# Kernel optimization log

Measured on AMD Instinct MI355X. Metric: run time of the kernel, lower is better.

## Reference

```python
import jax, jax.numpy as jnp
import numpy as np

D = 1024
H = 16
DH = D // H
SCALE = 1.0 / float(np.sqrt(DH))
EPS = 1e-5


def layer_norm(x, g, b):
    mu = jnp.mean(x, axis=-1, keepdims=True)
    var = jnp.mean((x - mu) ** 2, axis=-1, keepdims=True)
    return (x - mu) * jax.lax.rsqrt(var + EPS) * g + b


def setup_inputs() -> dict:
    key = jax.random.key(0)
    ks = jax.random.split(key, 12)
    B, N = 2, 2048
    x = jax.random.normal(ks[0], (B, N, D), dtype=jnp.float32)
    # sparse 0/1 adjacency (tree-like density) plus self loops
    adj = (jax.random.uniform(ks[1], (B, N, N)) < 0.002).astype(jnp.float32)
    adj = jnp.maximum(adj, jnp.eye(N, dtype=jnp.float32)[None])
    attn_mask = jnp.zeros((B, N, N), dtype=jnp.float32)
    s = 0.02
    params = {
        "qkv_w": jax.random.normal(ks[2], (D, 3 * D)) * s,
        "qkv_b": jnp.zeros((3 * D,), jnp.float32),
        "out_w": jax.random.normal(ks[3], (D, D)) * s,
        "out_b": jnp.zeros((D,), jnp.float32),
        "ln1_g": jnp.ones((D,), jnp.float32),
        "ln1_b": jnp.zeros((D,), jnp.float32),
        "ln2_g": jnp.ones((D,), jnp.float32),
        "ln2_b": jnp.zeros((D,), jnp.float32),
        "ff1_w": jax.random.normal(ks[4], (D, 4 * D)) * s,
        "ff1_b": jnp.zeros((4 * D,), jnp.float32),
        "ff2_w": jax.random.normal(ks[5], (4 * D, D)) * s,
        "ff2_b": jnp.zeros((D,), jnp.float32),
        "struct_bias": jnp.zeros((1,), jnp.float32) + 0.1,
    }
    return {"x": x, "adjacency": adj, "attn_mask": attn_mask, **params}


def reference(x, adjacency, attn_mask, qkv_w, qkv_b, out_w, out_b,
              ln1_g, ln1_b, ln2_g, ln2_b, ff1_w, ff1_b, ff2_w, ff2_b,
              struct_bias):
    b, n, d = x.shape
    residual = x
    h = layer_norm(x, ln1_g, ln1_b)
    qkv = (h @ qkv_w + qkv_b).reshape(b, n, 3, H, DH)
    q = jnp.transpose(qkv[:, :, 0], (0, 2, 1, 3))  # [B,H,N,Dh]
    k = jnp.transpose(qkv[:, :, 1], (0, 2, 1, 3))
    v = jnp.transpose(qkv[:, :, 2], (0, 2, 1, 3))
    scores = jnp.einsum("bhqd,bhkd->bhqk", q, k) * SCALE
    scores = scores + struct_bias[0] * adjacency[:, None] + attn_mask[:, None]
    attn = jax.nn.softmax(scores, axis=-1)  # dropout is identity at eval
    out = jnp.einsum("bhqk,bhkd->bhqd", attn, v)
    out = jnp.transpose(out, (0, 2, 1, 3)).reshape(b, n, d)
    out = out @ out_w + out_b
    x1 = residual + out
    h2 = layer_norm(x1, ln2_g, ln2_b)
    ff = jax.nn.gelu(h2 @ ff1_w + ff1_b, approximate=False) @ ff2_w + ff2_b
    return x1 + ff
```

## Files before the change

kernel.cpp:

```cpp
#include <hip/hip_runtime.h>
#include <math.h>

#define Dm 1024
#define Hh 16
#define DHh 64
#define Bb 2
#define Nn 2048
#define Rr 4096
#define SCALE_ 0.125f
#define EPS_ 1e-5f
#define SMAX_ 4.0f
#define LOG2E_ 1.4426950408889634f

typedef unsigned short u16;
typedef __attribute__((ext_vector_type(8))) short short8;
typedef __attribute__((ext_vector_type(4))) float f32x4;

__device__ __forceinline__ u16 f2bf(float f) {
  union { float f; unsigned u; } v; v.f = f;
  unsigned r = v.u + 0x7fffu + ((v.u >> 16) & 1u);
  return (u16)(r >> 16);
}
__device__ __forceinline__ u16 f2bf_t(float f) {
  union { float f; unsigned u; } v; v.f = f;
  return (u16)(v.u >> 16);
}
__device__ __forceinline__ float bf2f(u16 h) {
  union { unsigned u; float f; } v; v.u = ((unsigned)h) << 16;
  return v.f;
}

__device__ __forceinline__ void g2l16(const u16* g, const u16* l) {
  __builtin_amdgcn_global_load_lds(
      (const __attribute__((address_space(1))) void*)g,
      (__attribute__((address_space(3))) void*)l, 16, 0, 0);
}

__global__ void transpose_to_bf16(const float* __restrict__ W, u16* __restrict__ WT,
                                  int K, int N) {
  __shared__ float tile[32][33];
  int n0 = blockIdx.x * 32, k0 = blockIdx.y * 32;
  int tx = threadIdx.x, ty = threadIdx.y;
#pragma unroll
  for (int i = 0; i < 4; i++)
    tile[ty + 8 * i][tx] = W[(size_t)(k0 + ty + 8 * i) * N + n0 + tx];
  __syncthreads();
#pragma unroll
  for (int i = 0; i < 4; i++)
    WT[(size_t)(n0 + ty + 8 * i) * K + k0 + tx] = f2bf(tile[tx][ty + 8 * i]);
}

__global__ void bias_precompute(const float* __restrict__ adj, const float* __restrict__ mask,
                                const float* __restrict__ sbp, u16* __restrict__ bias16) {
  const float sb = sbp[0];
  size_t i = ((size_t)blockIdx.x * 256 + threadIdx.x) * 8;
  float4 a0 = *(const float4*)(adj + i);
  float4 a1 = *(const float4*)(adj + i + 4);
  float4 m0 = *(const float4*)(mask + i);
  float4 m1 = *(const float4*)(mask + i + 4);
  ushort4 o0, o1;
  o0.x = f2bf(sb * a0.x + m0.x); o0.y = f2bf(sb * a0.y + m0.y);
  o0.z = f2bf(sb * a0.z + m0.z); o0.w = f2bf(sb * a0.w + m0.w);
  o1.x = f2bf(sb * a1.x + m1.x); o1.y = f2bf(sb * a1.y + m1.y);
  o1.z = f2bf(sb * a1.z + m1.z); o1.w = f2bf(sb * a1.w + m1.w);
  *(ushort4*)(bias16 + i) = o0;
  *(ushort4*)(bias16 + i + 4) = o1;
}

template <int BI>
__global__ void ln_kernel(const void* __restrict__ xin, const float* __restrict__ g,
                          const float* __restrict__ be, u16* __restrict__ out) {
  int row = blockIdx.x;
  int t = threadIdx.x;
  float4 v;
  if (BI) {
    ushort4 uv = ((const ushort4*)((const u16*)xin + (size_t)row * Dm))[t];
    v.x = bf2f(uv.x); v.y = bf2f(uv.y); v.z = bf2f(uv.z); v.w = bf2f(uv.w);
  } else {
    v = ((const float4*)((const float*)xin + (size_t)row * Dm))[t];
  }
  float s = v.x + v.y + v.z + v.w;
  float s2 = v.x * v.x + v.y * v.y + v.z * v.z + v.w * v.w;
#pragma unroll
  for (int o = 32; o > 0; o >>= 1) { s += __shfl_down(s, o); s2 += __shfl_down(s2, o); }
  __shared__ float sm[8];
  int w = t >> 6;
  if ((t & 63) == 0) { sm[w] = s; sm[4 + w] = s2; }
  __syncthreads();
  if (t == 0) {
    float a = sm[0] + sm[1] + sm[2] + sm[3];
    float a2 = sm[4] + sm[5] + sm[6] + sm[7];
    float mu = a * (1.f / Dm);
    sm[0] = mu;
    sm[1] = rsqrtf(a2 * (1.f / Dm) - mu * mu + EPS_);
  }
  __syncthreads();
  float mu = sm[0], rstd = sm[1];
  float4 gv = ((const float4*)g)[t];
  float4 bv = ((const float4*)be)[t];
  ushort4 o4;
  o4.x = f2bf((v.x - mu) * rstd * gv.x + bv.x);
  o4.y = f2bf((v.y - mu) * rstd * gv.y + bv.y);
  o4.z = f2bf((v.z - mu) * rstd * gv.z + bv.z);
  o4.w = f2bf((v.w - mu) * rstd * gv.w + bv.w);
  ((ushort4*)(out + (size_t)row * Dm))[t] = o4;
}

template <int MODE, int MI, int NI>
__global__ __launch_bounds__(256) void gemm_bt(
    const u16* __restrict__ A, const u16* __restrict__ BT,
    const float* __restrict__ bias, const void* __restrict__ res,
    void* __restrict__ Cout, u16* __restrict__ qb,
    u16* __restrict__ kb, u16* __restrict__ vb, int Ndim, int Kdim) {
  constexpr int TM = MI * 32, TN = NI * 32;
  constexpr int NS = (TM + TN) / 16;
  __shared__ u16 As[2][TM * 32];
  __shared__ u16 Bs[2][TN * 32];
  const int t = threadIdx.x;
  const int wave = t >> 6, lane = t & 63;
  const int wm = wave >> 1, wn = wave & 1;
  const int lr = lane & 15, lq = lane >> 4;
  const int flat = blockIdx.x + gridDim.x * blockIdx.y;
  constexpr int nMb = 4096 / TM;
  constexpr int mpx = nMb / 8;
  const int xcd = flat & 7;
  const int p = flat >> 3;
  const int m0 = (xcd * mpx + (p % mpx)) * TM;
  const int n0 = (p / mpx) * TN;

  auto stage = [&](int kt, int bsel) {
    for (int s = wave; s < NS; s += 4) {
      if (s < TM / 16)
        g2l16(A + (size_t)(m0 + s * 16 + (lane >> 2)) * Kdim + kt + (lane & 3) * 8,
              &As[bsel][(s * 16) * 32]);
      else
        g2l16(BT + (size_t)(n0 + (s - TM / 16) * 16 + (lane >> 2)) * Kdim + kt + (lane & 3) * 8,
              &Bs[bsel][((s - TM / 16) * 16) * 32]);
    }
  };

  f32x4 acc[MI][NI];
#pragma unroll
  for (int i = 0; i < MI; i++)
#pragma unroll
    for (int j = 0; j < NI; j++) acc[i][j] = (f32x4){0.f, 0.f, 0.f, 0.f};

  stage(0, 0);
  int cur = 0;
  for (int kt = 0; kt < Kdim; kt += 32) {
    __syncthreads();
    if (kt + 32 < Kdim) stage(kt + 32, cur ^ 1);
    short8 af[MI], bf[NI];
#pragma unroll
    for (int i = 0; i < MI; i++)
      af[i] = *(const short8*)&As[cur][(wm * (MI * 16) + i * 16 + lr) * 32 + lq * 8];
#pragma unroll
    for (int j = 0; j < NI; j++)
      bf[j] = *(const short8*)&Bs[cur][(wn * (NI * 16) + j * 16 + lr) * 32 + lq * 8];
#pragma unroll
    for (int i = 0; i < MI; i++)
#pragma unroll
      for (int j = 0; j < NI; j++)
        acc[i][j] = __builtin_amdgcn_mfma_f32_16x16x32_bf16(af[i], bf[j], acc[i][j], 0, 0, 0);
    cur ^= 1;
  }

#pragma unroll
  for (int i = 0; i < MI; i++) {
#pragma unroll
    for (int j = 0; j < NI; j++) {
#pragma unroll
      for (int r = 0; r < 4; r++) {
        int row = m0 + wm * (MI * 16) + i * 16 + lq * 4 + r;
        int col = n0 + wn * (NI * 16) + j * 16 + lr;
        float val = acc[i][j][r] + bias[col];
        if (MODE == 0) {
          int s = col >> 10, rem = col & 1023;
          int hh = rem >> 6, dh = rem & 63;
          int bi = row >> 11, ni = row & 2047;
          if (s == 2) {
            vb[(((size_t)bi * Hh + hh) * DHh + dh) * Nn + ni] = f2bf(val);
          } else {
            u16* dst = (s == 0) ? qb : kb;
            dst[(((size_t)bi * Hh + hh) * Nn + ni) * DHh + dh] = f2bf(val);
          }
        } else if (MODE == 1) {
          size_t o = (size_t)row * Ndim + col;
          ((u16*)Cout)[o] = f2bf(val + ((const float*)res)[o]);
        } else if (MODE == 3) {
          size_t o = (size_t)row * Ndim + col;
          ((float*)Cout)[o] = val + bf2f(((const u16*)res)[o]);
        } else {
          size_t o = (size_t)row * Ndim + col;
          float gv = 0.5f * val * (1.f + erff(val * 0.70710678118f));
          ((u16*)Cout)[o] = f2bf(gv);
        }
      }
    }
  }
}

__global__ __launch_bounds__(256) void attn_kernel(
    const u16* __restrict__ q, const u16* __restrict__ k, const u16* __restrict__ vT,
    const u16* __restrict__ bias16, u16* __restrict__ out) {
  const int qt = blockIdx.x, hb = blockIdx.y;
  const int hh = hb & 15, b = hb >> 4;
  const int t = threadIdx.x, wave = t >> 6, lane = t & 63;
  const int lr = lane & 15, lq = lane >> 4;
  const size_t head_off = (((size_t)b * Hh + hh) * Nn) * DHh;
  const u16* Q = q + head_off;
  const u16* K = k + head_off;
  const u16* Vt = vT + head_off;
  const int q0 = qt * 128;

  __shared__ u16 Ks[64 * 72];
  __shared__ u16 VsT[64 * 72];
  __shared__ u16 Ps[4][32 * 72];

  short8 qf[2][2];
#pragma unroll
  for (int qs = 0; qs < 2; qs++) {
    const u16* Qr = Q + (size_t)(q0 + wave * 32 + qs * 16 + lr) * DHh;
    qf[qs][0] = *(const short8*)(Qr + lq * 8);
    qf[qs][1] = *(const short8*)(Qr + 32 + lq * 8);
  }
  f32x4 o_acc[2][4];
  float l_acc[2][4];
#pragma unroll
  for (int qs = 0; qs < 2; qs++) {
#pragma unroll
    for (int j = 0; j < 4; j++) o_acc[qs][j] = (f32x4){0.f, 0.f, 0.f, 0.f};
#pragma unroll
    for (int r = 0; r < 4; r++) l_acc[qs][r] = 0.f;
  }

  const int srow = t >> 2;
  const int sc0 = (t & 3) * 16;
  const int ssw = ((srow >> 2) & 3) << 4;
  const int wc0 = sc0 ^ ssw, wc1 = (sc0 + 8) ^ ssw;
  const u16* Kst = K + (size_t)srow * DHh + sc0;
  const u16* Vst = Vt + (size_t)srow * Nn + sc0;
  const int rsw = ((lr >> 2) & 3) << 4;

  const u16* bp = bias16 + ((size_t)b * Nn + q0 + wave * 32 + lq * 4) * Nn + lr;

  f32x4 kr0 = *(const f32x4*)(Kst);
  f32x4 kr1 = *(const f32x4*)(Kst + 8);
  f32x4 vr0 = *(const f32x4*)(Vst);
  f32x4 vr1 = *(const f32x4*)(Vst + 8);
  unsigned short bw[2][4][4];
#pragma unroll
  for (int qs = 0; qs < 2; qs++)
#pragma unroll
    for (int ns = 0; ns < 4; ns++)
#pragma unroll
      for (int r = 0; r < 4; r++)
        bw[qs][ns][r] = bp[(size_t)(qs * 16 + r) * Nn + ns * 16];

  const float C1 = SCALE_ * LOG2E_;
  const float C3 = -SMAX_ * LOG2E_;

  for (int kt = 0; kt < Nn; kt += 64) {
    __syncthreads();
    *(f32x4*)&Ks[srow * 72 + wc0] = kr0;
    *(f32x4*)&Ks[srow * 72 + wc1] = kr1;
    *(f32x4*)&VsT[srow * 72 + wc0] = vr0;
    *(f32x4*)&VsT[srow * 72 + wc1] = vr1;
    __syncthreads();
    if (kt + 64 < Nn) {
      kr0 = *(const f32x4*)(Kst + (size_t)(kt + 64) * DHh);
      kr1 = *(const f32x4*)(Kst + (size_t)(kt + 64) * DHh + 8);
      vr0 = *(const f32x4*)(Vst + kt + 64);
      vr1 = *(const f32x4*)(Vst + kt + 64 + 8);
    }
    short8 kf[4][2];
#pragma unroll
    for (int ns = 0; ns < 4; ns++) {
      int row = ns * 16 + lr;
      kf[ns][0] = *(const short8*)&Ks[row * 72 + ((lq * 8) ^ rsw)];
      kf[ns][1] = *(const short8*)&Ks[row * 72 + ((32 + lq * 8) ^ rsw)];
    }
    f32x4 s0[4], s1[4];
#pragma unroll
    for (int ns = 0; ns < 4; ns++) {
      s0[ns] = (f32x4){0.f, 0.f, 0.f, 0.f};
      s1[ns] = (f32x4){0.f, 0.f, 0.f, 0.f};
      s0[ns] = __builtin_amdgcn_mfma_f32_16x16x32_bf16(qf[0][0], kf[ns][0], s0[ns], 0, 0, 0);
      s0[ns] = __builtin_amdgcn_mfma_f32_16x16x32_bf16(qf[0][1], kf[ns][1], s0[ns], 0, 0, 0);
      s1[ns] = __builtin_amdgcn_mfma_f32_16x16x32_bf16(qf[1][0], kf[ns][0], s1[ns], 0, 0, 0);
      s1[ns] = __builtin_amdgcn_mfma_f32_16x16x32_bf16(qf[1][1], kf[ns][1], s1[ns], 0, 0, 0);
    }
    float p0[4][4], p1[4][4];
#pragma unroll
    for (int ns = 0; ns < 4; ns++)
#pragma unroll
      for (int r = 0; r < 4; r++) {
        p0[ns][r] = exp2f(fmaf(s0[ns][r], C1, fmaf(bf2f(bw[0][ns][r]), LOG2E_, C3)));
        p1[ns][r] = exp2f(fmaf(s1[ns][r], C1, fmaf(bf2f(bw[1][ns][r]), LOG2E_, C3)));
        l_acc[0][r] += p0[ns][r];
        l_acc[1][r] += p1[ns][r];
      }
    if (kt + 64 < Nn) {
#pragma unroll
      for (int qs = 0; qs < 2; qs++)
#pragma unroll
        for (int ns = 0; ns < 4; ns++)
#pragma unroll
          for (int r = 0; r < 4; r++)
            bw[qs][ns][r] = bp[(size_t)(qs * 16 + r) * Nn + kt + 64 + ns * 16];
    }
#pragma unroll
    for (int ns = 0; ns < 4; ns++) {
      int csw = ((ns ^ lq) << 4) + lr;
#pragma unroll
      for (int r = 0; r < 4; r++) {
        Ps[wave][(lq * 4 + r) * 72 + csw] = f2bf_t(p0[ns][r]);
        Ps[wave][(16 + lq * 4 + r) * 72 + csw] = f2bf_t(p1[ns][r]);
      }
    }
    short8 pf[2][2];
#pragma unroll
    for (int qs = 0; qs < 2; qs++) {
      pf[qs][0] = *(const short8*)&Ps[wave][(qs * 16 + lr) * 72 + ((lq * 8) ^ rsw)];
      pf[qs][1] = *(const short8*)&Ps[wave][(qs * 16 + lr) * 72 + ((32 + lq * 8) ^ rsw)];
    }
#pragma unroll
    for (int j = 0; j < 4; j++) {
      int row = j * 16 + lr;
      short8 vf0 = *(const short8*)&VsT[row * 72 + ((lq * 8) ^ rsw)];
      short8 vf1 = *(const short8*)&VsT[row * 72 + ((32 + lq * 8) ^ rsw)];
      o_acc[0][j] = __builtin_amdgcn_mfma_f32_16x16x32_bf16(pf[0][0], vf0, o_acc[0][j], 0, 0, 0);
      o_acc[0][j] = __builtin_amdgcn_mfma_f32_16x16x32_bf16(pf[0][1], vf1, o_acc[0][j], 0, 0, 0);
      o_acc[1][j] = __builtin_amdgcn_mfma_f32_16x16x32_bf16(pf[1][0], vf0, o_acc[1][j], 0, 0, 0);
      o_acc[1][j] = __builtin_amdgcn_mfma_f32_16x16x32_bf16(pf[1][1], vf1, o_acc[1][j], 0, 0, 0);
    }
  }
#pragma unroll
  for (int qs = 0; qs < 2; qs++)
#pragma unroll
    for (int r = 0; r < 4; r++) {
#pragma unroll
      for (int o = 1; o < 16; o <<= 1) l_acc[qs][r] += __shfl_xor(l_acc[qs][r], o);
      float inv = 1.0f / l_acc[qs][r];
      int qrow = q0 + wave * 32 + qs * 16 + lq * 4 + r;
#pragma unroll
      for (int j = 0; j < 4; j++) {
        out[((size_t)(b * Nn + qrow)) * Dm + hh * DHh + j * 16 + lr] =
            f2bf(o_acc[qs][j][r] * inv);
      }
    }
}

extern "C" void kernel_launch(void* const* d_in, const int* in_sizes, int n_in,
                              void* d_out, int out_size, void* d_ws, size_t ws_size,
                              hipStream_t stream) {
  const float* x     = (const float*)d_in[0];
  const float* adj   = (const float*)d_in[1];
  const float* amask = (const float*)d_in[2];
  const float* qkv_w = (const float*)d_in[3];
  const float* qkv_b = (const float*)d_in[4];
  const float* out_w = (const float*)d_in[5];
  const float* out_b = (const float*)d_in[6];
  const float* ln1_g = (const float*)d_in[7];
  const float* ln1_b = (const float*)d_in[8];
  const float* ln2_g = (const float*)d_in[9];
  const float* ln2_b = (const float*)d_in[10];
  const float* ff1_w = (const float*)d_in[11];
  const float* ff1_b = (const float*)d_in[12];
  const float* ff2_w = (const float*)d_in[13];
  const float* ff2_b = (const float*)d_in[14];
  const float* sbias = (const float*)d_in[15];

  char* w = (char*)d_ws;
  const size_t MB = 1024 * 1024;
  u16* h      = (u16*)(w);
  u16* qb     = (u16*)(w + 8 * MB);
  u16* kb     = (u16*)(w + 16 * MB);
  u16* vb     = (u16*)(w + 24 * MB);
  u16* ao     = (u16*)(w + 32 * MB);
  u16* x1     = (u16*)(w + 40 * MB);
  u16* qkvT   = (u16*)(w + 56 * MB);
  u16* outT   = (u16*)(w + 62 * MB);
  u16* ff1T   = (u16*)(w + 64 * MB);
  u16* ff2T   = (u16*)(w + 72 * MB);
  u16* bias16 = (u16*)(w + 80 * MB);
  u16* ffo    = qb;

  transpose_to_bf16<<<dim3(3072 / 32, 1024 / 32), dim3(32, 8), 0, stream>>>(qkv_w, qkvT, 1024, 3072);
  transpose_to_bf16<<<dim3(1024 / 32, 1024 / 32), dim3(32, 8), 0, stream>>>(out_w, outT, 1024, 1024);
  transpose_to_bf16<<<dim3(4096 / 32, 1024 / 32), dim3(32, 8), 0, stream>>>(ff1_w, ff1T, 1024, 4096);
  transpose_to_bf16<<<dim3(1024 / 32, 4096 / 32), dim3(32, 8), 0, stream>>>(ff2_w, ff2T, 4096, 1024);

  bias_precompute<<<dim3((Bb * Nn * Nn) / (8 * 256)), dim3(256), 0, stream>>>(adj, amask, sbias, bias16);

  ln_kernel<0><<<dim3(Rr), dim3(256), 0, stream>>>(x, ln1_g, ln1_b, h);

  gemm_bt<0, 4, 4><<<dim3(3072 / 128, 4096 / 128), dim3(256), 0, stream>>>(
      h, qkvT, qkv_b, nullptr, nullptr, qb, kb, vb, 3072, 1024);

  attn_kernel<<<dim3(16, 32), dim3(256), 0, stream>>>(qb, kb, vb, bias16, ao);

  gemm_bt<1, 2, 2><<<dim3(1024 / 64, 4096 / 64), dim3(256), 0, stream>>>(
      ao, outT, out_b, x, (void*)x1, nullptr, nullptr, nullptr, 1024, 1024);

  ln_kernel<1><<<dim3(Rr), dim3(256), 0, stream>>>(x1, ln2_g, ln2_b, h);

  gemm_bt<2, 4, 4><<<dim3(4096 / 128, 4096 / 128), dim3(256), 0, stream>>>(
      h, ff1T, ff1_b, nullptr, (void*)ffo, nullptr, nullptr, nullptr, 4096, 1024);

  gemm_bt<3, 2, 2><<<dim3(1024 / 64, 4096 / 64), dim3(256), 0, stream>>>(
      ffo, ff2T, ff2_b, x1, d_out, nullptr, nullptr, nullptr, 1024, 4096);
}
```

Before: 495.2 us.

## Split attention over key halves, merge weight transposes, use tanh-form GELU

Attention now splits the key dimension into two halves across a third grid axis. Each half writes unnormalised bf16 partial outputs and row sums, and a new combine kernel adds them and normalises. This doubles the attention block count for better occupancy on the GPU, at the cost of extra global traffic and bf16 rounding of the partials. The four weight-transpose launches are merged into one. The erf GELU is replaced by a tanh-style sigmoid approximation using __expf, which changes numerics. A staging loop also gets an unroll pragma.

```diff
diff --git a/kernel.cpp b/kernel.cpp
--- a/kernel.cpp
+++ b/kernel.cpp
@@ -36,10 +36,19 @@
       (__attribute__((address_space(3))) void*)l, 16, 0, 0);
 }
 
-__global__ void transpose_to_bf16(const float* __restrict__ W, u16* __restrict__ WT,
-                                  int K, int N) {
+__global__ void transpose_all(const float* __restrict__ qkv_w, const float* __restrict__ out_w,
+                              const float* __restrict__ ff1_w, const float* __restrict__ ff2_w,
+                              u16* __restrict__ qkvT, u16* __restrict__ outT,
+                              u16* __restrict__ ff1T, u16* __restrict__ ff2T) {
   __shared__ float tile[32][33];
-  int n0 = blockIdx.x * 32, k0 = blockIdx.y * 32;
+  int flat = blockIdx.x;
+  const float* W; u16* WT; int K, N, local;
+  if (flat < 3072)        { W = qkv_w; WT = qkvT; K = 1024; N = 3072; local = flat; }
+  else if (flat < 4096)   { W = out_w; WT = outT; K = 1024; N = 1024; local = flat - 3072; }
+  else if (flat < 8192)   { W = ff1_w; WT = ff1T; K = 1024; N = 4096; local = flat - 4096; }
+  else                    { W = ff2_w; WT = ff2T; K = 4096; N = 1024; local = flat - 8192; }
+  int nx = N / 32;
+  int n0 = (local % nx) * 32, k0 = (local / nx) * 32;
   int tx = threadIdx.x, ty = threadIdx.y;
 #pragma unroll
   for (int i = 0; i < 4; i++)
@@ -129,6 +138,7 @@
   const int n0 = (p / mpx) * TN;
 
   auto stage = [&](int kt, int bsel) {
+#pragma unroll
     for (int s = wave; s < NS; s += 4) {
       if (s < TM / 16)
         g2l16(A + (size_t)(m0 + s * 16 + (lane >> 2)) * Kdim + kt + (lane & 3) * 8,
@@ -191,8 +201,10 @@
           size_t o = (size_t)row * Ndim + col;
           ((float*)Cout)[o] = val + bf2f(((const u16*)res)[o]);
         } else {
+          float u = val;
+          float y2 = 1.5957691216f * fmaf(0.044715f * u, u * u, u);
+          float gv = u / (1.f + __expf(-y2));
           size_t o = (size_t)row * Ndim + col;
-          float gv = 0.5f * val * (1.f + erff(val * 0.70710678118f));
           ((u16*)Cout)[o] = f2bf(gv);
         }
       }
@@ -202,8 +214,9 @@
 
 __global__ __launch_bounds__(256) void attn_kernel(
     const u16* __restrict__ q, const u16* __restrict__ k, const u16* __restrict__ vT,
-    const u16* __restrict__ bias16, u16* __restrict__ out) {
-  const int qt = blockIdx.x, hb = blockIdx.y;
+    const u16* __restrict__ bias16, u16* __restrict__ pO0, u16* __restrict__ pO1,
+    float* __restrict__ pl) {
+  const int qt = blockIdx.x, hb = blockIdx.y, kp = blockIdx.z;
   const int hh = hb & 15, b = hb >> 4;
   const int t = threadIdx.x, wave = t >> 6, lane = t & 63;
   const int lr = lane & 15, lq = lane >> 4;
@@ -212,6 +225,8 @@
   const u16* K = k + head_off;
   const u16* Vt = vT + head_off;
   const int q0 = qt * 128;
+  const int kbase = kp * (Nn / 2);
+  u16* pO = kp ? pO1 : pO0;
 
   __shared__ u16 Ks[64 * 72];
   __shared__ u16 VsT[64 * 72];
@@ -244,10 +259,10 @@
 
   const u16* bp = bias16 + ((size_t)b * Nn + q0 + wave * 32 + lq * 4) * Nn + lr;
 
-  f32x4 kr0 = *(const f32x4*)(Kst);
-  f32x4 kr1 = *(const f32x4*)(Kst + 8);
-  f32x4 vr0 = *(const f32x4*)(Vst);
-  f32x4 vr1 = *(const f32x4*)(Vst + 8);
+  f32x4 kr0 = *(const f32x4*)(Kst + (size_t)kbase * DHh);
+  f32x4 kr1 = *(const f32x4*)(Kst + (size_t)kbase * DHh + 8);
+  f32x4 vr0 = *(const f32x4*)(Vst + kbase);
+  f32x4 vr1 = *(const f32x4*)(Vst + kbase + 8);
   unsigned short bw[2][4][4];
 #pragma unroll
   for (int qs = 0; qs < 2; qs++)
@@ -255,19 +270,20 @@
     for (int ns = 0; ns < 4; ns++)
 #pragma unroll
       for (int r = 0; r < 4; r++)
-        bw[qs][ns][r] = bp[(size_t)(qs * 16 + r) * Nn + ns * 16];
+        bw[qs][ns][r] = bp[(size_t)(qs * 16 + r) * Nn + kbase + ns * 16];
 
   const float C1 = SCALE_ * LOG2E_;
   const float C3 = -SMAX_ * LOG2E_;
-
-  for (int kt = 0; kt < Nn; kt += 64) {
+  const int kend = kbase + Nn / 2;
+
+  for (int kt = kbase; kt < kend; kt += 64) {
     __syncthreads();
     *(f32x4*)&Ks[srow * 72 + wc0] = kr0;
     *(f32x4*)&Ks[srow * 72 + wc1] = kr1;
     *(f32x4*)&VsT[srow * 72 + wc0] = vr0;
     *(f32x4*)&VsT[srow * 72 + wc1] = vr1;
     __syncthreads();
-    if (kt + 64 < Nn) {
+    if (kt + 64 < kend) {
       kr0 = *(const f32x4*)(Kst + (size_t)(kt + 64) * DHh);
       kr1 = *(const f32x4*)(Kst + (size_t)(kt + 64) * DHh + 8);
       vr0 = *(const f32x4*)(Vst + kt + 64);
@@ -300,7 +316,7 @@
         l_acc[0][r] += p0[ns][r];
         l_acc[1][r] += p1[ns][r];
       }
-    if (kt + 64 < Nn) {
+    if (kt + 64 < kend) {
 #pragma unroll
       for (int qs = 0; qs < 2; qs++)
 #pragma unroll
@@ -341,14 +357,33 @@
     for (int r = 0; r < 4; r++) {
 #pragma unroll
       for (int o = 1; o < 16; o <<= 1) l_acc[qs][r] += __shfl_xor(l_acc[qs][r], o);
-      float inv = 1.0f / l_acc[qs][r];
       int qrow = q0 + wave * 32 + qs * 16 + lq * 4 + r;
+      if (lr == 0)
+        pl[((size_t)(kp * Bb + b) * Hh + hh) * Nn + qrow] = l_acc[qs][r];
 #pragma unroll
       for (int j = 0; j < 4; j++) {
-        out[((size_t)(b * Nn + qrow)) * Dm + hh * DHh + j * 16 + lr] =
-            f2bf(o_acc[qs][j][r] * inv);
+        pO[((size_t)(b * Nn + qrow)) * Dm + hh * DHh + j * 16 + lr] =
+            f2bf(o_acc[qs][j][r]);
       }
     }
+}
+
+__global__ void attn_combine(const u16* __restrict__ pO0, const u16* __restrict__ pO1,
+                             const float* __restrict__ pl, u16* __restrict__ ao) {
+  int row = blockIdx.x;
+  int t = threadIdx.x;
+  int col = t * 4;
+  int b = row >> 11, n = row & 2047, hh = col >> 6;
+  size_t li = ((size_t)b * Hh + hh) * Nn + n;
+  float inv = 1.f / (pl[li] + pl[(size_t)Bb * Hh * Nn + li]);
+  ushort4 a0 = *(const ushort4*)(pO0 + (size_t)row * Dm + col);
+  ushort4 a1 = *(const ushort4*)(pO1 + (size_t)row * Dm + col);
+  ushort4 o;
+  o.x = f2bf((bf2f(a0.x) + bf2f(a1.x)) * inv);
+  o.y = f2bf((bf2f(a0.y) + bf2f(a1.y)) * inv);
+  o.z = f2bf((bf2f(a0.z) + bf2f(a1.z)) * inv);
+  o.w = f2bf((bf2f(a0.w) + bf2f(a1.w)) * inv);
+  *(ushort4*)(ao + (size_t)row * Dm + col) = o;
 }
 
 extern "C" void kernel_launch(void* const* d_in, const int* in_sizes, int n_in,
@@ -378,7 +413,10 @@
   u16* kb     = (u16*)(w + 16 * MB);
   u16* vb     = (u16*)(w + 24 * MB);
   u16* ao     = (u16*)(w + 32 * MB);
+  float* pl   = (float*)(w + 40 * MB);
   u16* x1     = (u16*)(w + 40 * MB);
+  u16* pO0    = (u16*)(w + 48 * MB);
+  u16* pO1    = h;
   u16* qkvT   = (u16*)(w + 56 * MB);
   u16* outT   = (u16*)(w + 62 * MB);
   u16* ff1T   = (u16*)(w + 64 * MB);
@@ -386,10 +424,8 @@
   u16* bias16 = (u16*)(w + 80 * MB);
   u16* ffo    = qb;
 
-  transpose_to_bf16<<<dim3(3072 / 32, 1024 / 32), dim3(32, 8), 0, stream>>>(qkv_w, qkvT, 1024, 3072);
-  transpose_to_bf16<<<dim3(1024 / 32, 1024 / 32), dim3(32, 8), 0, stream>>>(out_w, outT, 1024, 1024);
-  transpose_to_bf16<<<dim3(4096 / 32, 1024 / 32), dim3(32, 8), 0, stream>>>(ff1_w, ff1T, 1024, 4096);
-  transpose_to_bf16<<<dim3(1024 / 32, 4096 / 32), dim3(32, 8), 0, stream>>>(ff2_w, ff2T, 4096, 1024);
+  transpose_all<<<dim3(12288), dim3(32, 8), 0, stream>>>(
+      qkv_w, out_w, ff1_w, ff2_w, qkvT, outT, ff1T, ff2T);
 
   bias_precompute<<<dim3((Bb * Nn * Nn) / (8 * 256)), dim3(256), 0, stream>>>(adj, amask, sbias, bias16);
 
@@ -398,7 +434,9 @@
   gemm_bt<0, 4, 4><<<dim3(3072 / 128, 4096 / 128), dim3(256), 0, stream>>>(
       h, qkvT, qkv_b, nullptr, nullptr, qb, kb, vb, 3072, 1024);
 
-  attn_kernel<<<dim3(16, 32), dim3(256), 0, stream>>>(qb, kb, vb, bias16, ao);
+  attn_kernel<<<dim3(16, 32, 2), dim3(256), 0, stream>>>(qb, kb, vb, bias16, pO0, pO1, pl);
+
+  attn_combine<<<dim3(Rr), dim3(256), 0, stream>>>(pO0, pO1, pl, ao);
 
   gemm_bt<1, 2, 2><<<dim3(1024 / 64, 4096 / 64), dim3(256), 0, stream>>>(
       ao, outT, out_b, x, (void*)x1, nullptr, nullptr, nullptr, 1024, 1024);
```

Measured after the change: 453.3 us. -8.5%, faster.
